# Optimization experiments

Measured on AMD Instinct MI355X. Metric: run time of the kernel, lower is better.

Reference implementation:

```python
import jax, jax.numpy as jnp
import numpy as np

B, V_IN, V_OUT, C_IN, C_OUT, K, NNZ = 16, 1024, 4096, 128, 256, 18, 16384

def setup_inputs() -> dict:
    key = jax.random.key(0)
    ks = jax.random.split(key, 10)
    def lin(k, fan_in, fan_out):
        s = 1.0 / np.sqrt(fan_in)
        return jax.random.normal(k, (fan_in, fan_out), jnp.float32) * s
    return {
        "x": jax.random.normal(ks[0], (B, V_IN, C_IN), jnp.float32),
        "vals": jax.random.uniform(ks[1], (NNZ,), jnp.float32),
        "W1": lin(ks[2], 1 * C_IN, C_OUT),
        "b1": jnp.zeros((C_OUT,), jnp.float32),
        "Wd3": lin(ks[3], (K // 3) * C_IN, C_OUT // 4),
        "bd3": jnp.zeros((C_OUT // 4,), jnp.float32),
        "W2d3": lin(ks[4], (K // 3 * 2) * C_IN, C_OUT // 4),
        "b2d3": jnp.zeros((C_OUT // 4,), jnp.float32),
        "Wf": lin(ks[5], K * C_IN, C_OUT // 2),
        "bf": jnp.zeros((C_OUT // 2,), jnp.float32),
        "rows": jax.random.randint(ks[6], (NNZ,), 0, V_OUT, jnp.int32),
        "cols": jax.random.randint(ks[7], (NNZ,), 0, V_IN, jnp.int32),
        "spiral_idx": jax.random.randint(ks[8], (V_OUT, K), 0, V_OUT, jnp.int32),
    }

def _pool(x, rows, cols, vals, dim_size):
    # sparse upsample: gather cols, scale, scatter-add to rows
    gathered = x[:, cols, :] * vals[None, :, None]  # [B, nnz, C]
    return jnp.zeros((x.shape[0], dim_size, x.shape[2]), x.dtype).at[:, rows, :].add(gathered)

def _spiral_conv(feat, idx, W, b):
    # gather fixed spiral neighborhoods then shared linear layer
    Bz, V, C = feat.shape[0], idx.shape[0], feat.shape[2]
    g = feat[:, idx.reshape(-1), :].reshape(Bz, V, idx.shape[1] * C)  # [B, V, K*C]
    return g @ W + b

def reference(x, vals, W1, b1, Wd3, bd3, W2d3, b2d3, Wf, bf, rows, cols, spiral_idx):
    out = _pool(x, rows, cols, vals, V_OUT)  # [B, V_OUT, C_IN]
    k = spiral_idx.shape[1]
    short_cut = _spiral_conv(out, spiral_idx[:, :1], W1, b1)
    p_d3 = _spiral_conv(out, spiral_idx[:, : k // 3], Wd3, bd3)
    p_2d3 = _spiral_conv(out, spiral_idx[:, : k // 3 * 2], W2d3, b2d3)
    p = _spiral_conv(out, spiral_idx, Wf, bf)
    f = jnp.concatenate((p, p_2d3, p_d3), axis=2)  # [B, V_OUT, C_OUT]
    return jax.nn.relu(short_cut + f)
```

## Files before the change

### kernel.cpp

```cpp
#include <hip/hip_runtime.h>
#include <hip/hip_bf16.h>

#define B_SZ   16
#define V_IN   1024
#define V_OUT  4096
#define C_IN   128
#define C_OUT  256
#define K_NB   18
#define NNZ    16384
#define K_GEMM (K_NB * C_IN)
#define BK     64
#define NKT    (K_GEMM / BK)

typedef __attribute__((ext_vector_type(8))) short bf16x8;
typedef __attribute__((ext_vector_type(4))) float f32x4;

#define GLOAD16(src, dst) __builtin_amdgcn_global_load_lds( \
    (const __attribute__((address_space(1))) unsigned int*)(src), \
    (__attribute__((address_space(3))) unsigned int*)(dst), 16, 0, 0)

#define MFMA16(a_, b_, c_) __builtin_amdgcn_mfma_f32_16x16x32_bf16((a_), (b_), (c_), 0, 0, 0)

__global__ __launch_bounds__(1024) void csr_kernel(const int* __restrict__ rows,
                                                   int* __restrict__ offsets,
                                                   int* __restrict__ perm) {
    __shared__ int cnt[V_OUT];
    __shared__ int wsum[16];
    const int t = threadIdx.x;
    const int lane = t & 63, wid = t >> 6;
#pragma unroll
    for (int i = t; i < V_OUT; i += 1024) cnt[i] = 0;
    __syncthreads();
#pragma unroll
    for (int n = t; n < NNZ; n += 1024) atomicAdd(&cnt[rows[n]], 1);
    __syncthreads();
    const int base4 = t * 4;
    int c0 = cnt[base4], c1 = cnt[base4 + 1], c2 = cnt[base4 + 2], c3 = cnt[base4 + 3];
    int tot = c0 + c1 + c2 + c3;
    int v = tot;
#pragma unroll
    for (int d = 1; d < 64; d <<= 1) {
        int u = __shfl_up(v, d);
        if (lane >= d) v += u;
    }
    if (lane == 63) wsum[wid] = v;
    __syncthreads();
    int wbase = 0;
#pragma unroll
    for (int w = 0; w < 16; ++w) wbase += (w < wid) ? wsum[w] : 0;
    int incl = wbase + v;
    int excl = incl - tot;
    offsets[base4]     = excl;
    offsets[base4 + 1] = excl + c0;
    offsets[base4 + 2] = excl + c0 + c1;
    offsets[base4 + 3] = excl + c0 + c1 + c2;
    if (t == 1023) offsets[V_OUT] = incl;
    __syncthreads();
    cnt[base4]     = excl;
    cnt[base4 + 1] = excl + c0;
    cnt[base4 + 2] = excl + c0 + c1;
    cnt[base4 + 3] = excl + c0 + c1 + c2;
    __syncthreads();
#pragma unroll
    for (int n = t; n < NNZ; n += 1024) {
        int pos = atomicAdd(&cnt[rows[n]], 1);
        perm[pos] = n;
    }
}

__global__ __launch_bounds__(512) void pool_kernel(
    const float* __restrict__ x, const float* __restrict__ vals,
    const int* __restrict__ cols, const int* __restrict__ offsets,
    const int* __restrict__ perm, __hip_bfloat16* __restrict__ pool) {
    int r = blockIdx.x;
    int t = threadIdx.x;
    int b = t >> 5, c4 = t & 31;
    int j0 = offsets[r], j1 = offsets[r + 1];
    const float4* xb = (const float4*)x + (size_t)b * (V_IN * 32);
    float4 acc = {0.f, 0.f, 0.f, 0.f};
    for (int j = j0; j < j1; ++j) {
        int n = perm[j];
        float v = vals[n];
        float4 xv = xb[cols[n] * 32 + c4];
        acc.x += v * xv.x; acc.y += v * xv.y; acc.z += v * xv.z; acc.w += v * xv.w;
    }
    ushort4 o;
    o.x = __builtin_bit_cast(unsigned short, __float2bfloat16(acc.x));
    o.y = __builtin_bit_cast(unsigned short, __float2bfloat16(acc.y));
    o.z = __builtin_bit_cast(unsigned short, __float2bfloat16(acc.z));
    o.w = __builtin_bit_cast(unsigned short, __float2bfloat16(acc.w));
    ((ushort4*)pool)[((size_t)b * V_OUT + r) * 32 + c4] = o;
}

__global__ void wcomb_kernel(const float* __restrict__ W1, const float* __restrict__ Wd3,
                             const float* __restrict__ W2d3, const float* __restrict__ Wf,
                             const float* __restrict__ b1, const float* __restrict__ bd3,
                             const float* __restrict__ b2d3, const float* __restrict__ bf,
                             __hip_bfloat16* __restrict__ wTs, float* __restrict__ bias) {
    int idx = blockIdx.x * blockDim.x + threadIdx.x;
    if (idx >= NKT * 16384) {
        int c = idx - NKT * 16384;
        if (c < C_OUT) {
            float v = b1[c];
            if (c < 128)      v += bf[c];
            else if (c < 192) v += b2d3[c - 128];
            else              v += bd3[c - 192];
            bias[c] = v;
        }
        return;
    }
    int kt = idx >> 14;
    int c  = (idx >> 3) & 2047;
    int e  = idx & 7;
    int nrow  = c >> 3;
    int kslot = (c & 7) << 4;
    int kb = kslot ^ ((nrow & 7) << 4);
    int r  = kt * 64 + (kb >> 1) + e;
    int col = nrow;
    float v;
    if (col < 128)      v = Wf[r * 128 + col];
    else if (col < 192) v = (r < 1536) ? W2d3[r * 64 + (col - 128)] : 0.f;
    else                v = (r < 768)  ? Wd3[r * 64 + (col - 192)]  : 0.f;
    if (r < 128) v += W1[r * 256 + col];
    wTs[idx] = __float2bfloat16(v);
}

__global__ __launch_bounds__(512, 4) void gemm_kernel(
    const __hip_bfloat16* __restrict__ pool,
    const __hip_bfloat16* __restrict__ wTs,
    const float* __restrict__ bias,
    const int* __restrict__ spiral,
    float* __restrict__ out)
{
    __shared__ __align__(16) char smem[53760];
    unsigned short* spl = (unsigned short*)(smem + 49152);

    const int tid  = threadIdx.x;
    const int lane = tid & 63;
    const int wid  = tid >> 6;
    const int q    = wid & 3;
    const int wmL  = (wid >> 2) << 6;

    const int bid = blockIdx.x;
    const int bm  = ((bid & 7) << 6) + (bid >> 3);
    const int b   = bm >> 5;
    const int v0  = (bm & 31) << 7;

    for (int i = tid; i < 128 * K_NB; i += 512)
        spl[i] = (unsigned short)spiral[(v0 + i / K_NB) * K_NB + (i % K_NB)];
    asm volatile("s_waitcnt vmcnt(0) lgkmcnt(0)" ::: "memory");
    __builtin_amdgcn_s_barrier();

    const char* poolBytes = (const char*)(pool + (size_t)b * V_OUT * C_IN);
    const char* wTsBytes  = (const char*)wTs;
    const int sb = ((tid & 7) << 4) ^ (((tid >> 3) & 7) << 4);

    auto stageA = [&](int kt, int slot) {
        const int j   = kt >> 1;
        const int c0b = (kt & 1) << 7;
        char* dst = smem + slot * 16384;
#pragma unroll
        for (int ch = 0; ch < 2; ++ch) {
            int flat = (ch << 9) + tid;
            int sidx = spl[(flat >> 3) * K_NB + j];
            GLOAD16(poolBytes + ((size_t)sidx << 8) + (c0b + sb), dst + (flat << 4));
        }
    };

    const int l15   = lane & 15;
    const int swm   = (lane & 7) << 4;
    const int klane = (lane >> 4) << 4;
    const int kk0   = klane ^ swm;
    const int kk1   = (64 + klane) ^ swm;
    const int aBase = (wmL + l15) << 7;
    const int bO0 = (((2 * q)     << 4) + l15) << 7;
    const int bO1 = (((2 * q + 1) << 4) + l15) << 7;
    const int bO2 = (((8 + q)     << 4) + l15) << 7;
    const int bO3 = (((12 + q)    << 4) + l15) << 7;

    f32x4 acc[4][4] = {};

    stageA(0, 0);
    stageA(1, 1);

    int sl = 0;
    for (int kt = 0; kt < NKT; ++kt) {
        if (kt + 1 < NKT) asm volatile("s_waitcnt vmcnt(2)" ::: "memory");
        else              asm volatile("s_waitcnt vmcnt(0)" ::: "memory");
        __builtin_amdgcn_s_barrier();
        __builtin_amdgcn_sched_barrier(0);

        const char* As  = smem + sl * 16384;
        const char* wKt = wTsBytes + ((size_t)kt << 15);
        const bool doMid = kt < 24, doShort = kt < 12;
        bf16x8 a[4], b0, b1, b2, b3;

        b0 = *(const bf16x8*)(wKt + bO0 + kk0);
        b1 = *(const bf16x8*)(wKt + bO1 + kk0);
        if (doMid)   b2 = *(const bf16x8*)(wKt + bO2 + kk0);
        if (doShort) b3 = *(const bf16x8*)(wKt + bO3 + kk0);
#pragma unroll
        for (int mi = 0; mi < 4; ++mi)
            a[mi] = *(const bf16x8*)(As + aBase + (mi << 11) + kk0);
        __builtin_amdgcn_s_setprio(1);
#pragma unroll
        for (int mi = 0; mi < 4; ++mi) {
            acc[mi][0] = MFMA16(a[mi], b0, acc[mi][0]);
            acc[mi][1] = MFMA16(a[mi], b1, acc[mi][1]);
        }
        if (doMid) {
#pragma unroll
            for (int mi = 0; mi < 4; ++mi) acc[mi][2] = MFMA16(a[mi], b2, acc[mi][2]);
        }
        if (doShort) {
#pragma unroll
            for (int mi = 0; mi < 4; ++mi) acc[mi][3] = MFMA16(a[mi], b3, acc[mi][3]);
        }
        __builtin_amdgcn_s_setprio(0);

        b0 = *(const bf16x8*)(wKt + bO0 + kk1);
        b1 = *(const bf16x8*)(wKt + bO1 + kk1);
        if (doMid)   b2 = *(const bf16x8*)(wKt + bO2 + kk1);
        if (doShort) b3 = *(const bf16x8*)(wKt + bO3 + kk1);
#pragma unroll
        for (int mi = 0; mi < 4; ++mi)
            a[mi] = *(const bf16x8*)(As + aBase + (mi << 11) + kk1);
        __builtin_amdgcn_sched_barrier(0);
        if (kt + 2 < NKT) {
            int st = sl + 2; if (st >= 3) st -= 3;
            stageA(kt + 2, st);
        }
        __builtin_amdgcn_sched_barrier(0);
        __builtin_amdgcn_s_setprio(1);
#pragma unroll
        for (int mi = 0; mi < 4; ++mi) {
            acc[mi][0] = MFMA16(a[mi], b0, acc[mi][0]);
            acc[mi][1] = MFMA16(a[mi], b1, acc[mi][1]);
        }
        if (doMid) {
#pragma unroll
            for (int mi = 0; mi < 4; ++mi) acc[mi][2] = MFMA16(a[mi], b2, acc[mi][2]);
        }
        if (doShort) {
#pragma unroll
            for (int mi = 0; mi < 4; ++mi) acc[mi][3] = MFMA16(a[mi], b3, acc[mi][3]);
        }
        __builtin_amdgcn_s_setprio(0);

        sl += 1; if (sl >= 3) sl -= 3;
    }

    const int nt[4] = {2 * q, 2 * q + 1, 8 + q, 12 + q};
#pragma unroll
    for (int ni = 0; ni < 4; ++ni) {
        int col = (nt[ni] << 4) + l15;
        float bz = bias[col];
#pragma unroll
        for (int mi = 0; mi < 4; ++mi) {
            int row0 = v0 + wmL + mi * 16 + ((lane >> 4) << 2);
#pragma unroll
            for (int r4 = 0; r4 < 4; ++r4) {
                float v = acc[mi][ni][r4] + bz;
                out[((size_t)(b * V_OUT + row0 + r4)) * C_OUT + col] = v > 0.f ? v : 0.f;
            }
        }
    }
}

extern "C" void kernel_launch(void* const* d_in, const int* in_sizes, int n_in,
                              void* d_out, int out_size, void* d_ws, size_t ws_size,
                              hipStream_t stream) {
    const float* x     = (const float*)d_in[0];
    const float* vals  = (const float*)d_in[1];
    const float* W1    = (const float*)d_in[2];
    const float* b1    = (const float*)d_in[3];
    const float* Wd3   = (const float*)d_in[4];
    const float* bd3   = (const float*)d_in[5];
    const float* W2d3  = (const float*)d_in[6];
    const float* b2d3  = (const float*)d_in[7];
    const float* Wf    = (const float*)d_in[8];
    const float* bf    = (const float*)d_in[9];
    const int*   rows  = (const int*)d_in[10];
    const int*   cols  = (const int*)d_in[11];
    const int*   spiral= (const int*)d_in[12];
    float* out = (float*)d_out;

    char* ws = (char*)d_ws;
    __hip_bfloat16* pool = (__hip_bfloat16*)ws;
    __hip_bfloat16* wTs  = (__hip_bfloat16*)(ws + 16777216);
    float* bias          = (float*)(ws + 16777216 + 1179648);
    int*   offsets       = (int*)(ws + 16777216 + 1179648 + 1024);
    int*   perm          = offsets + V_OUT + 4;

    csr_kernel<<<1, 1024, 0, stream>>>(rows, offsets, perm);
    pool_kernel<<<V_OUT, 512, 0, stream>>>(x, vals, cols, offsets, perm, pool);
    wcomb_kernel<<<(NKT * 16384 + C_OUT + 255) / 256, 256, 0, stream>>>(
        W1, Wd3, W2d3, Wf, b1, bd3, b2d3, bf, wTs, bias);
    gemm_kernel<<<512, 512, 0, stream>>>(pool, wTs, bias, spiral, out);
}
```

Measured before the change: 121.1 us.

## Double tile height per block and stage Wf weight columns through LDS

The GEMM block grows to 1024 threads covering 256 vertices instead of 128, so each block does twice the work and the grid is halved. The Wf weight columns are now staged into LDS with a double-buffered async load, rather than every wave reading them from global memory. The A gather moves from a 3-slot to a 2-slot ring with an extra barrier per iteration, and the spiral index table is kept as int. Shared memory rises to about 114 KB, which allows only one block per CU and reduces latency hiding. The tighter pipeline also adds synchronisation.

```diff
diff --git a/kernel.cpp b/kernel.cpp
--- a/kernel.cpp
+++ b/kernel.cpp
@@ -125,29 +125,28 @@
     wTs[idx] = __float2bfloat16(v);
 }
 
-__global__ __launch_bounds__(512, 4) void gemm_kernel(
+__global__ __launch_bounds__(1024, 4) void gemm_kernel(
     const __hip_bfloat16* __restrict__ pool,
     const __hip_bfloat16* __restrict__ wTs,
     const float* __restrict__ bias,
     const int* __restrict__ spiral,
     float* __restrict__ out)
 {
-    __shared__ __align__(16) char smem[53760];
-    unsigned short* spl = (unsigned short*)(smem + 49152);
+    __shared__ __align__(16) char smem[116736];
+    int* spl = (int*)(smem + 98304);
 
     const int tid  = threadIdx.x;
     const int lane = tid & 63;
     const int wid  = tid >> 6;
-    const int q    = wid & 3;
-    const int wmL  = (wid >> 2) << 6;
+    const int wc   = wid & 3;
+    const int wm   = (wid >> 2) << 6;
 
     const int bid = blockIdx.x;
-    const int bm  = ((bid & 7) << 6) + (bid >> 3);
-    const int b   = bm >> 5;
-    const int v0  = (bm & 31) << 7;
-
-    for (int i = tid; i < 128 * K_NB; i += 512)
-        spl[i] = (unsigned short)spiral[(v0 + i / K_NB) * K_NB + (i % K_NB)];
+    const int bm  = ((bid & 7) << 5) + (bid >> 3);
+    const int b   = bm >> 4;
+    const int v0  = (bm & 15) << 8;
+
+    for (int i = tid; i < 256 * K_NB; i += 1024) spl[i] = spiral[v0 * K_NB + i];
     asm volatile("s_waitcnt vmcnt(0) lgkmcnt(0)" ::: "memory");
     __builtin_amdgcn_s_barrier();
 
@@ -155,16 +154,22 @@
     const char* wTsBytes  = (const char*)wTs;
     const int sb = ((tid & 7) << 4) ^ (((tid >> 3) & 7) << 4);
 
-    auto stageA = [&](int kt, int slot) {
+    auto stageA = [&](int kt) {
         const int j   = kt >> 1;
         const int c0b = (kt & 1) << 7;
-        char* dst = smem + slot * 16384;
+        char* dst = smem + ((kt & 1) << 15);
 #pragma unroll
         for (int ch = 0; ch < 2; ++ch) {
-            int flat = (ch << 9) + tid;
+            int flat = (ch << 10) + tid;
             int sidx = spl[(flat >> 3) * K_NB + j];
-            GLOAD16(poolBytes + ((size_t)sidx << 8) + (c0b + sb), dst + (flat << 4));
-        }
+            GLOAD16(poolBytes + ((size_t)sidx << 8) + (c0b + sb), dst + flat * 16);
+        }
+    };
+    auto stageB = [&](int kt) {
+        const char* src = wTsBytes + ((size_t)kt << 15);
+        char* dst = smem + 65536 + ((kt & 1) << 14);
+        int off = tid << 4;
+        GLOAD16(src + off, dst + off);
     };
 
     const int l15   = lane & 15;
@@ -172,92 +177,124 @@
     const int klane = (lane >> 4) << 4;
     const int kk0   = klane ^ swm;
     const int kk1   = (64 + klane) ^ swm;
-    const int aBase = (wmL + l15) << 7;
-    const int bO0 = (((2 * q)     << 4) + l15) << 7;
-    const int bO1 = (((2 * q + 1) << 4) + l15) << 7;
-    const int bO2 = (((8 + q)     << 4) + l15) << 7;
-    const int bO3 = (((12 + q)    << 4) + l15) << 7;
+    const int aBase = (wm + l15) << 7;
+    const int bOff0 = (((2 * wc)     << 4) + l15) << 7;
+    const int bOff1 = (((2 * wc + 1) << 4) + l15) << 7;
+    const int bOff2 = (((8 + wc)     << 4) + l15) << 7;
+    const int bOff3 = (((12 + wc)    << 4) + l15) << 7;
 
     f32x4 acc[4][4] = {};
 
-    stageA(0, 0);
-    stageA(1, 1);
-
-    int sl = 0;
+    stageA(0);
+    stageB(0);
+
     for (int kt = 0; kt < NKT; ++kt) {
-        if (kt + 1 < NKT) asm volatile("s_waitcnt vmcnt(2)" ::: "memory");
-        else              asm volatile("s_waitcnt vmcnt(0)" ::: "memory");
+        const int s = kt & 1;
+        const char* As = smem + (s << 15);
+        const char* Bs = smem + 65536 + (s << 14);
+        const char* wKt = wTsBytes + ((size_t)kt << 15);
+
+        if (kt + 1 < NKT) {
+            stageA(kt + 1);
+            asm volatile("s_waitcnt vmcnt(2)" ::: "memory");
+        } else {
+            asm volatile("s_waitcnt vmcnt(0)" ::: "memory");
+        }
         __builtin_amdgcn_s_barrier();
         __builtin_amdgcn_sched_barrier(0);
 
-        const char* As  = smem + sl * 16384;
-        const char* wKt = wTsBytes + ((size_t)kt << 15);
-        const bool doMid = kt < 24, doShort = kt < 12;
-        bf16x8 a[4], b0, b1, b2, b3;
-
-        b0 = *(const bf16x8*)(wKt + bO0 + kk0);
-        b1 = *(const bf16x8*)(wKt + bO1 + kk0);
-        if (doMid)   b2 = *(const bf16x8*)(wKt + bO2 + kk0);
-        if (doShort) b3 = *(const bf16x8*)(wKt + bO3 + kk0);
-#pragma unroll
-        for (int mi = 0; mi < 4; ++mi)
-            a[mi] = *(const bf16x8*)(As + aBase + (mi << 11) + kk0);
-        __builtin_amdgcn_s_setprio(1);
-#pragma unroll
-        for (int mi = 0; mi < 4; ++mi) {
-            acc[mi][0] = MFMA16(a[mi], b0, acc[mi][0]);
-            acc[mi][1] = MFMA16(a[mi], b1, acc[mi][1]);
-        }
-        if (doMid) {
-#pragma unroll
-            for (int mi = 0; mi < 4; ++mi) acc[mi][2] = MFMA16(a[mi], b2, acc[mi][2]);
-        }
-        if (doShort) {
-#pragma unroll
-            for (int mi = 0; mi < 4; ++mi) acc[mi][3] = MFMA16(a[mi], b3, acc[mi][3]);
-        }
-        __builtin_amdgcn_s_setprio(0);
-
-        b0 = *(const bf16x8*)(wKt + bO0 + kk1);
-        b1 = *(const bf16x8*)(wKt + bO1 + kk1);
-        if (doMid)   b2 = *(const bf16x8*)(wKt + bO2 + kk1);
-        if (doShort) b3 = *(const bf16x8*)(wKt + bO3 + kk1);
-#pragma unroll
-        for (int mi = 0; mi < 4; ++mi)
-            a[mi] = *(const bf16x8*)(As + aBase + (mi << 11) + kk1);
+        const bool doMid   = kt < 24;
+        const bool doShort = kt < 12;
+
+        bf16x8 g20, g21, g30, g31;
+        if (doMid)   { g20 = *(const bf16x8*)(wKt + bOff2 + kk0);
+                       g21 = *(const bf16x8*)(wKt + bOff2 + kk1); }
+        if (doShort) { g30 = *(const bf16x8*)(wKt + bOff3 + kk0);
+                       g31 = *(const bf16x8*)(wKt + bOff3 + kk1); }
+
+        {
+            bf16x8 a0 = *(const bf16x8*)(As + aBase + (0 << 11) + kk0);
+            bf16x8 a1 = *(const bf16x8*)(As + aBase + (1 << 11) + kk0);
+            bf16x8 a2 = *(const bf16x8*)(As + aBase + (2 << 11) + kk0);
+            bf16x8 a3 = *(const bf16x8*)(As + aBase + (3 << 11) + kk0);
+            bf16x8 bb0 = *(const bf16x8*)(Bs + bOff0 + kk0);
+            bf16x8 bb1 = *(const bf16x8*)(Bs + bOff1 + kk0);
+            __builtin_amdgcn_s_setprio(1);
+            acc[0][0] = MFMA16(a0, bb0, acc[0][0]);
+            acc[1][0] = MFMA16(a1, bb0, acc[1][0]);
+            acc[2][0] = MFMA16(a2, bb0, acc[2][0]);
+            acc[3][0] = MFMA16(a3, bb0, acc[3][0]);
+            acc[0][1] = MFMA16(a0, bb1, acc[0][1]);
+            acc[1][1] = MFMA16(a1, bb1, acc[1][1]);
+            acc[2][1] = MFMA16(a2, bb1, acc[2][1]);
+            acc[3][1] = MFMA16(a3, bb1, acc[3][1]);
+            __builtin_amdgcn_s_setprio(0);
+            if (doMid) {
+                __builtin_amdgcn_s_setprio(1);
+                acc[0][2] = MFMA16(a0, g20, acc[0][2]);
+                acc[1][2] = MFMA16(a1, g20, acc[1][2]);
+                acc[2][2] = MFMA16(a2, g20, acc[2][2]);
+                acc[3][2] = MFMA16(a3, g20, acc[3][2]);
+                __builtin_amdgcn_s_setprio(0);
+            }
+            if (doShort) {
+                __builtin_amdgcn_s_setprio(1);
+                acc[0][3] = MFMA16(a0, g30, acc[0][3]);
+                acc[1][3] = MFMA16(a1, g30, acc[1][3]);
+                acc[2][3] = MFMA16(a2, g30, acc[2][3]);
+                acc[3][3] = MFMA16(a3, g30, acc[3][3]);
+                __builtin_amdgcn_s_setprio(0);
+            }
+            if (kt + 1 < NKT) stageB(kt + 1);
+        }
+
+        {
+            bf16x8 a0 = *(const bf16x8*)(As + aBase + (0 << 11) + kk1);
+            bf16x8 a1 = *(const bf16x8*)(As + aBase + (1 << 11) + kk1);
+            bf16x8 a2 = *(const bf16x8*)(As + aBase + (2 << 11) + kk1);
+            bf16x8 a3 = *(const bf16x8*)(As + aBase + (3 << 11) + kk1);
+            bf16x8 bb0 = *(const bf16x8*)(Bs + bOff0 + kk1);
+            bf16x8 bb1 = *(const bf16x8*)(Bs + bOff1 + kk1);
+            __builtin_amdgcn_s_setprio(1);
+            acc[0][0] = MFMA16(a0, bb0, acc[0][0]);
+            acc[1][0] = MFMA16(a1, bb0, acc[1][0]);
+            acc[2][0] = MFMA16(a2, bb0, acc[2][0]);
+            acc[3][0] = MFMA16(a3, bb0, acc[3][0]);
+            acc[0][1] = MFMA16(a0, bb1, acc[0][1]);
+            acc[1][1] = MFMA16(a1, bb1, acc[1][1]);
+            acc[2][1] = MFMA16(a2, bb1, acc[2][1]);
+            acc[3][1] = MFMA16(a3, bb1, acc[3][1]);
+            __builtin_amdgcn_s_setprio(0);
+            if (doMid) {
+                __builtin_amdgcn_s_setprio(1);
+                acc[0][2] = MFMA16(a0, g21, acc[0][2]);
+                acc[1][2] = MFMA16(a1, g21, acc[1][2]);
+                acc[2][2] = MFMA16(a2, g21, acc[2][2]);
+                acc[3][2] = MFMA16(a3, g21, acc[3][2]);
+                __builtin_amdgcn_s_setprio(0);
+            }
+            if (doShort) {
+                __builtin_amdgcn_s_setprio(1);
+                acc[0][3] = MFMA16(a0, g31, acc[0][3]);
+                acc[1][3] = MFMA16(a1, g31, acc[1][3]);
+                acc[2][3] = MFMA16(a2, g31, acc[2][3]);
+                acc[3][3] = MFMA16(a3, g31, acc[3][3]);
+                __builtin_amdgcn_s_setprio(0);
+            }
+        }
+
+        __builtin_amdgcn_s_barrier();
         __builtin_amdgcn_sched_barrier(0);
-        if (kt + 2 < NKT) {
-            int st = sl + 2; if (st >= 3) st -= 3;
-            stageA(kt + 2, st);
-        }
-        __builtin_amdgcn_sched_barrier(0);
-        __builtin_amdgcn_s_setprio(1);
-#pragma unroll
-        for (int mi = 0; mi < 4; ++mi) {
-            acc[mi][0] = MFMA16(a[mi], b0, acc[mi][0]);
-            acc[mi][1] = MFMA16(a[mi], b1, acc[mi][1]);
-        }
-        if (doMid) {
-#pragma unroll
-            for (int mi = 0; mi < 4; ++mi) acc[mi][2] = MFMA16(a[mi], b2, acc[mi][2]);
-        }
-        if (doShort) {
-#pragma unroll
-            for (int mi = 0; mi < 4; ++mi) acc[mi][3] = MFMA16(a[mi], b3, acc[mi][3]);
-        }
-        __builtin_amdgcn_s_setprio(0);
-
-        sl += 1; if (sl >= 3) sl -= 3;
-    }
-
-    const int nt[4] = {2 * q, 2 * q + 1, 8 + q, 12 + q};
+    }
+
+    const int nt[4] = {2 * wc, 2 * wc + 1, 8 + wc, 12 + wc};
 #pragma unroll
     for (int ni = 0; ni < 4; ++ni) {
         int col = (nt[ni] << 4) + l15;
         float bz = bias[col];
 #pragma unroll
         for (int mi = 0; mi < 4; ++mi) {
-            int row0 = v0 + wmL + mi * 16 + ((lane >> 4) << 2);
+            int row0 = v0 + wm + mi * 16 + ((lane >> 4) << 2);
 #pragma unroll
             for (int r4 = 0; r4 < 4; ++r4) {
                 float v = acc[mi][ni][r4] + bz;
@@ -296,5 +333,5 @@
     pool_kernel<<<V_OUT, 512, 0, stream>>>(x, vals, cols, offsets, perm, pool);
     wcomb_kernel<<<(NKT * 16384 + C_OUT + 255) / 256, 256, 0, stream>>>(
         W1, Wd3, W2d3, Wf, b1, bd3, b2d3, bf, wTs, bias);
-    gemm_kernel<<<512, 512, 0, stream>>>(pool, wTs, bias, spiral, out);
-}
+    gemm_kernel<<<256, 1024, 0, stream>>>(pool, wTs, bias, spiral, out);
+}
```

Result: no change. 122.0 us (+0.8%).
